# Optimization experiments

Measured on AMD Instinct MI355X. Metric: run time of the kernel, lower is better.

Reference implementation:

```python
import jax, jax.numpy as jnp
import numpy as np
from jax import lax

# sRGB linear -> LMS matrix (Oklab M1)
M1 = jnp.array([[0.4122214708, 0.5363325363, 0.0514459929],
                [0.2119034982, 0.6806995451, 0.1073969566],
                [0.0883024619, 0.2817188376, 0.6299787005]], dtype=jnp.float32)
# LMS^(1/3) -> Oklab matrix (Oklab M2)
M2 = jnp.array([[0.2104542553, 0.7936177850, -0.0040720468],
                [1.9779984951, -2.4285922050, 0.4505937099],
                [0.0259040371, 0.7827717662, -0.8086757660]], dtype=jnp.float32)
_SX = jnp.array([[-1., 0., 1.], [-2., 0., 2.], [-1., 0., 1.]], dtype=jnp.float32)
_SY = jnp.array([[-1., -2., -1.], [0., 0., 0.], [1., 2., 1.]], dtype=jnp.float32)
SOBEL = jnp.stack([_SX, _SY])[:, None]  # (2,1,3,3) cross-correlation kernels

CLOSING_KERNEL = 11
CLOSING_PAD = CLOSING_KERNEL // 2
EDGE_THRESHOLD = 0.5
POST_DILATION = 2
EPS = 0.01


def _srgb_to_linear(srgb):
    srgb = jnp.clip(srgb, 0.0, 1.0)
    return jnp.where(srgb <= 0.04045, srgb / 12.92, ((srgb + 0.055) / 1.055) ** 2.4)


def _rgb_to_oklab(rgb):  # [B,3,H,W] -> [B,3,H,W]
    linear = _srgb_to_linear(rgb)
    lms = jnp.einsum('oc,bchw->bohw', M1, linear)
    lms = jnp.clip(lms, 1e-10, None) ** (1.0 / 3.0)
    return jnp.einsum('oc,bchw->bohw', M2, lms)


def _max_pool(x, k, p):  # torch max_pool2d pads with -inf implicitly
    return lax.reduce_window(x, -jnp.inf, lax.max, (1, 1, k, k), (1, 1, 1, 1),
                             [(0, 0), (0, 0), (p, p), (p, p)])


def _min_pool(x, k, p):  # -max_pool(-x): padding becomes +inf
    return lax.reduce_window(x, jnp.inf, lax.min, (1, 1, k, k), (1, 1, 1, 1),
                             [(0, 0), (0, 0), (p, p), (p, p)])


def _omni_edge(img):  # [B,C,H,W] -> [B,1,H,W]
    B, C, H, W = img.shape
    flat = img.reshape(B * C, 1, H, W)
    g = lax.conv_general_dilated(flat, SOBEL, (1, 1), [(1, 1), (1, 1)])  # [B*C,2,H,W]
    grad = (jnp.abs(g[:, 0]) + jnp.abs(g[:, 1])).reshape(B, C, H, W)
    return jnp.max(grad, axis=1, keepdims=True)


def _crevice_mask(target):
    edge_soft = jnp.clip(_omni_edge(target) / EDGE_THRESHOLD, 0.0, 1.0)
    dilated = _max_pool(edge_soft, CLOSING_KERNEL, CLOSING_PAD)
    closed = _min_pool(dilated, CLOSING_KERNEL, CLOSING_PAD)
    mask = jax.nn.relu(closed - edge_soft)
    if POST_DILATION > 0:
        dk = 2 * POST_DILATION + 1
        mask = _max_pool(mask, dk, POST_DILATION)
    return mask


def setup_inputs() -> dict:
    key = jax.random.key(0)
    k1, k2 = jax.random.split(key)
    shape = (8, 3, 1024, 1024)
    pred = jax.random.uniform(k1, shape, dtype=jnp.float32)
    target = jax.random.uniform(k2, shape, dtype=jnp.float32)
    return {"pred": pred, "target": target}


def reference(pred, target):
    crevice_mask = _crevice_mask(target)
    mask_sum = jnp.maximum(crevice_mask.sum(), 1.0)
    pred_lab = _rgb_to_oklab(pred)
    target_lab = _rgb_to_oklab(target)
    p_a, p_b = pred_lab[:, 1:2], pred_lab[:, 2:3]
    t_a, t_b = target_lab[:, 1:2], target_lab[:, 2:3]
    C_pred = jnp.sqrt(p_a ** 2 + p_b ** 2 + 1e-12)
    C_gt = jnp.sqrt(t_a ** 2 + t_b ** 2 + 1e-12)
    chroma_loss = (jnp.abs(C_pred - C_gt) * crevice_mask).sum() / mask_sum
    dot_ab = p_a * t_a + p_b * t_b
    cos_hue_diff = jnp.clip(dot_ab / (C_pred * C_gt + 1e-12), -1.0, 1.0)
    hue_loss = (jnp.clip(C_gt, EPS, None) * (1.0 - cos_hue_diff) * crevice_mask).sum() / mask_sum
    return chroma_loss + 2.0 * hue_loss
```

## Files before the change

### kernel.cpp

```cpp
#include <hip/hip_runtime.h>
#include <math.h>

#define K1_NR 8
#define SROWS 64
#define PCH   16
#define QCAP  1024


__device__ __forceinline__ float srgb_to_linear(float x) {
    x = fminf(fmaxf(x, 0.0f), 1.0f);
    return (x <= 0.04045f) ? x * (1.0f / 12.92f)
                           : powf((x + 0.055f) * (1.0f / 1.055f), 2.4f);
}

__device__ __forceinline__ void oklab_ab(float r, float g, float b,
                                         float& A, float& Bc) {
    r = srgb_to_linear(r);
    g = srgb_to_linear(g);
    b = srgb_to_linear(b);
    float l = 0.4122214708f * r + 0.5363325363f * g + 0.0514459929f * b;
    float m = 0.2119034982f * r + 0.6806995451f * g + 0.1073969566f * b;
    float s = 0.0883024619f * r + 0.2817188376f * g + 0.6299787005f * b;
    l = cbrtf(fmaxf(l, 1e-10f));
    m = cbrtf(fmaxf(m, 1e-10f));
    s = cbrtf(fmaxf(s, 1e-10f));
    A  = 1.9779984951f * l - 2.428592205f * m + 0.4505937099f * s;
    Bc = 0.0259040371f * l + 0.7827717662f * m - 0.808675766f  * s;
}

__device__ __forceinline__ void color_terms(const float* __restrict__ pred,
                                            const float* __restrict__ target,
                                            size_t off, size_t HWp, float m,
                                            float& sc, float& sh) {
    float pa, pb, ta, tb;
    oklab_ab(pred[off], pred[off + HWp], pred[off + 2 * HWp], pa, pb);
    oklab_ab(target[off], target[off + HWp], target[off + 2 * HWp], ta, tb);
    float Cp = sqrtf(pa * pa + pb * pb + 1e-12f);
    float Cg = sqrtf(ta * ta + tb * tb + 1e-12f);
    sc += fabsf(Cp - Cg) * m;
    float cosd = (pa * ta + pb * tb) / (Cp * Cg + 1e-12f);
    cosd = fminf(fmaxf(cosd, -1.0f), 1.0f);
    sh += fmaxf(Cg, 0.01f) * (1.0f - cosd) * m;
}


__global__ __launch_bounds__(256) void k1_edge(const float* __restrict__ target,
                                               float* __restrict__ edge,
                                               int H, int W) {
    int strips = H / K1_NR;
    int b   = blockIdx.x / strips;
    int ysi = blockIdx.x % strips;
    int lane = threadIdx.x & 63, q = threadIdx.x >> 6;
    int col0 = (q << 8) + (lane << 2);
    int y0 = ysi * K1_NR;
    size_t HW = (size_t)H * W;
    const float* tb = target + (size_t)b * 3 * HW;
    float* ep = edge + (size_t)b * HW + col0;

    bool lok = (col0 > 0);
    bool rok = (col0 + 4 < W);
    int lc = lok ? col0 - 1 : 0;
    int rc = rok ? col0 + 4 : W - 1;

    float4 pr[3], cu[3], nx[3];
    float lpr[3], lcu[3], lnx[3], rpr[3], rcu[3], rnx[3];
#pragma unroll
    for (int c = 0; c < 3; ++c) {
        const float* p = tb + (size_t)c * HW;
        if (y0 > 0) {
            const float* r = p + (size_t)(y0 - 1) * W;
            pr[c]  = *(const float4*)(r + col0);
            lpr[c] = lok ? r[lc] : 0.f;
            rpr[c] = rok ? r[rc] : 0.f;
        } else {
            pr[c] = make_float4(0.f, 0.f, 0.f, 0.f);
            lpr[c] = 0.f; rpr[c] = 0.f;
        }
        const float* r = p + (size_t)y0 * W;
        cu[c]  = *(const float4*)(r + col0);
        lcu[c] = lok ? r[lc] : 0.f;
        rcu[c] = rok ? r[rc] : 0.f;
    }

#pragma unroll
    for (int y = y0; y < y0 + K1_NR; ++y) {
        bool okn = (y + 1 < H);
#pragma unroll
        for (int c = 0; c < 3; ++c) {
            const float* r = tb + (size_t)c * HW + (size_t)(y + 1) * W;
            nx[c]  = okn ? *(const float4*)(r + col0)
                         : make_float4(0.f, 0.f, 0.f, 0.f);
            lnx[c] = (okn && lok) ? r[lc] : 0.f;
            rnx[c] = (okn && rok) ? r[rc] : 0.f;
        }
        float4 g = make_float4(0.f, 0.f, 0.f, 0.f);
#pragma unroll
        for (int c = 0; c < 3; ++c) {
            float4 u, v;
            u.x = fmaf(2.f, cu[c].x, pr[c].x) + nx[c].x;
            u.y = fmaf(2.f, cu[c].y, pr[c].y) + nx[c].y;
            u.z = fmaf(2.f, cu[c].z, pr[c].z) + nx[c].z;
            u.w = fmaf(2.f, cu[c].w, pr[c].w) + nx[c].w;
            v.x = nx[c].x - pr[c].x;
            v.y = nx[c].y - pr[c].y;
            v.z = nx[c].z - pr[c].z;
            v.w = nx[c].w - pr[c].w;
            float ul = fmaf(2.f, lcu[c], lpr[c]) + lnx[c];
            float vl = lnx[c] - lpr[c];
            float ur = fmaf(2.f, rcu[c], rpr[c]) + rnx[c];
            float vr = rnx[c] - rpr[c];
            float4 gx, gy;
            gx.x = u.y - ul;  gx.y = u.z - u.x;
            gx.z = u.w - u.y; gx.w = ur - u.z;
            gy.x = fmaf(2.f, v.x, vl)  + v.y;
            gy.y = fmaf(2.f, v.y, v.x) + v.z;
            gy.z = fmaf(2.f, v.z, v.y) + v.w;
            gy.w = fmaf(2.f, v.w, v.z) + vr;
            g.x = fmaxf(g.x, fabsf(gx.x) + fabsf(gy.x));
            g.y = fmaxf(g.y, fabsf(gx.y) + fabsf(gy.y));
            g.z = fmaxf(g.z, fabsf(gx.z) + fabsf(gy.z));
            g.w = fmaxf(g.w, fabsf(gx.w) + fabsf(gy.w));
        }
        float4 e;
        e.x = fminf(2.f * g.x, 1.f);
        e.y = fminf(2.f * g.y, 1.f);
        e.z = fminf(2.f * g.z, 1.f);
        e.w = fminf(2.f * g.w, 1.f);
        *(float4*)(ep + (size_t)y * W) = e;
#pragma unroll
        for (int c = 0; c < 3; ++c) {
            pr[c] = cu[c];   cu[c] = nx[c];
            lpr[c] = lcu[c]; lcu[c] = lnx[c];
            rpr[c] = rcu[c]; rcu[c] = rnx[c];
        }
    }
}


template <int R, bool ISMAX, bool SUB_EDGE>
__global__ __launch_bounds__(256) void pool_kernel(const float* __restrict__ in,
                                                   const float* __restrict__ edge,
                                                   float* __restrict__ out,
                                                   int H, int W) {
    const int OUTW = 256 - 2 * R;
    __shared__ float s_v[PCH][256];
    int cb = (W + OUTW - 1) / OUTW;
    int rs = H / SROWS;
    int blk = blockIdx.x;
    int b   = blk / (cb * rs);
    int t   = blk % (cb * rs);
    int bxi = t / rs, ysi = t % rs;
    int tid = threadIdx.x;
    int col = bxi * OUTW - R + tid;
    int cc  = min(max(col, 0), W - 1);
    size_t base = (size_t)b * H * W;
    const float* colp = in + base + cc;
    int ys = ysi * SROWS;
    bool writer = (tid >= R) && (tid < OUTW + R) && (col < W);

    for (int ph = 0; ph < SROWS / PCH; ++ph) {
        int y0 = ys + ph * PCH;
        float w[PCH + 2 * R];
#pragma unroll
        for (int k = 0; k < PCH + 2 * R; ++k) {
            int r = min(max(y0 - R + k, 0), H - 1);
            w[k] = colp[(size_t)r * W];
        }
        float v[PCH];
#pragma unroll
        for (int k = 0; k < PCH; ++k) {
            float m = w[k];
#pragma unroll
            for (int d = 1; d <= 2 * R; ++d)
                m = ISMAX ? fmaxf(m, w[k + d]) : fminf(m, w[k + d]);
            v[k] = m;
        }
        __syncthreads();
#pragma unroll
        for (int k = 0; k < PCH; ++k) s_v[k][tid] = v[k];
        __syncthreads();
        if (writer) {
#pragma unroll
            for (int k = 0; k < PCH; ++k) {
                float m = s_v[k][tid - R];
#pragma unroll
                for (int d = 1; d <= 2 * R; ++d)
                    m = ISMAX ? fmaxf(m, s_v[k][tid - R + d])
                              : fminf(m, s_v[k][tid - R + d]);
                size_t gi = base + (size_t)(y0 + k) * W + col;
                out[gi] = SUB_EDGE ? fmaxf(m - edge[gi], 0.f) : m;
            }
        }
    }
}


__global__ __launch_bounds__(256) void k4_loss(const float* __restrict__ pred,
                                               const float* __restrict__ target,
                                               const float* __restrict__ mask0,
                                               float* __restrict__ partials,
                                               int H, int W, int nb) {
    const int R = 2, OUTW = 256 - 2 * R;
    __shared__ float s_v[PCH][256];
    __shared__ int   q_pos[QCAP];
    __shared__ float q_m[QCAP];
    __shared__ int   cnt;
    __shared__ float s_red[3][4];

    int cb = (W + OUTW - 1) / OUTW;
    int rs = H / SROWS;
    int blk = blockIdx.x;
    int b   = blk / (cb * rs);
    int t   = blk % (cb * rs);
    int bxi = t / rs, ysi = t % rs;
    int tid = threadIdx.x;
    int col = bxi * OUTW - R + tid;
    int cc  = min(max(col, 0), W - 1);
    size_t HWp  = (size_t)H * W;
    size_t base = (size_t)b * HWp;
    size_t cbase = (size_t)b * 3 * HWp;
    const float* colp = mask0 + base + cc;
    int ys = ysi * SROWS;
    bool writer = (tid >= R) && (tid < OUTW + R) && (col < W);

    float sm = 0.f, sc = 0.f, sh = 0.f;

    for (int ph = 0; ph < SROWS / PCH; ++ph) {
        int y0 = ys + ph * PCH;
        float w[PCH + 2 * R];
#pragma unroll
        for (int k = 0; k < PCH + 2 * R; ++k) {
            int r = min(max(y0 - R + k, 0), H - 1);
            w[k] = colp[(size_t)r * W];
        }
        float v[PCH];
#pragma unroll
        for (int k = 0; k < PCH; ++k) {
            float m = w[k];
#pragma unroll
            for (int d = 1; d <= 2 * R; ++d) m = fmaxf(m, w[k + d]);
            v[k] = m;
        }
        __syncthreads();
#pragma unroll
        for (int k = 0; k < PCH; ++k) s_v[k][tid] = v[k];
        if (tid == 0) cnt = 0;
        __syncthreads();
        if (writer) {
#pragma unroll
            for (int k = 0; k < PCH; ++k) {
                float m = s_v[k][tid - R];
#pragma unroll
                for (int d = 1; d <= 2 * R; ++d)
                    m = fmaxf(m, s_v[k][tid - R + d]);
                sm += m;
                if (m > 0.f) {
                    int pos = atomicAdd(&cnt, 1);
                    if (pos < QCAP) {
                        q_pos[pos] = ((y0 + k) << 16) | col;
                        q_m[pos] = m;
                    } else {
                        color_terms(pred, target,
                                    cbase + (size_t)(y0 + k) * W + col,
                                    HWp, m, sc, sh);
                    }
                }
            }
        }
        __syncthreads();
        int n = min(cnt, QCAP);
        for (int i = tid; i < n; i += 256) {
            int pk = q_pos[i];
            color_terms(pred, target,
                        cbase + (size_t)(pk >> 16) * W + (pk & 0xffff),
                        HWp, q_m[i], sc, sh);
        }
    }

#pragma unroll
    for (int off = 32; off > 0; off >>= 1) {
        sm += __shfl_down(sm, off);
        sc += __shfl_down(sc, off);
        sh += __shfl_down(sh, off);
    }
    int lane = tid & 63, wav = tid >> 6;
    __syncthreads();
    if (lane == 0) { s_red[0][wav] = sm; s_red[1][wav] = sc; s_red[2][wav] = sh; }
    __syncthreads();
    if (tid == 0) {
        float tm = 0, tc = 0, th = 0;
        for (int i = 0; i < 4; ++i) {
            tm += s_red[0][i]; tc += s_red[1][i]; th += s_red[2][i];
        }
        partials[blk]          = tm;
        partials[nb + blk]     = tc;
        partials[2 * nb + blk] = th;
    }
}

__global__ void finalize_kernel(const float* __restrict__ partials, int nb,
                                float* __restrict__ out) {
    double sm = 0.0, sc = 0.0, sh = 0.0;
    for (int i = threadIdx.x; i < nb; i += blockDim.x) {
        sm += (double)partials[i];
        sc += (double)partials[nb + i];
        sh += (double)partials[2 * nb + i];
    }
    __shared__ double red[3][256];
    red[0][threadIdx.x] = sm;
    red[1][threadIdx.x] = sc;
    red[2][threadIdx.x] = sh;
    __syncthreads();
    for (int s = blockDim.x / 2; s > 0; s >>= 1) {
        if ((int)threadIdx.x < s) {
            red[0][threadIdx.x] += red[0][threadIdx.x + s];
            red[1][threadIdx.x] += red[1][threadIdx.x + s];
            red[2][threadIdx.x] += red[2][threadIdx.x + s];
        }
        __syncthreads();
    }
    if (threadIdx.x == 0) {
        double ms = fmax(red[0][0], 1.0);
        out[0] = (float)(red[1][0] / ms + 2.0 * red[2][0] / ms);
    }
}


extern "C" void kernel_launch(void* const* d_in, const int* in_sizes, int n_in,
                              void* d_out, int out_size, void* d_ws, size_t ws_size,
                              hipStream_t stream) {
    const float* pred   = (const float*)d_in[0];
    const float* target = (const float*)d_in[1];
    float* out = (float*)d_out;

    const int H = 1024, W = 1024;
    int Bn = in_sizes[0] / (3 * H * W);
    size_t plane = (size_t)Bn * H * W * sizeof(float);

    char* ws = (char*)d_ws;
    float* planeA = (float*)ws;
    float* planeB = (float*)(ws + plane);
    float* partials = (float*)(ws + 2 * plane);

    int g1 = Bn * (H / K1_NR);
    int rs = H / SROWS;
    int cbP = (W + 245) / 246;
    int cb4 = (W + 251) / 252;
    int gP = Bn * cbP * rs;
    int g4 = Bn * cb4 * rs;

    k1_edge<<<g1, 256, 0, stream>>>(target, planeA, H, W);
    pool_kernel<5, true, false><<<gP, 256, 0, stream>>>(planeA, nullptr, planeB, H, W);
    pool_kernel<5, false, true><<<gP, 256, 0, stream>>>(planeB, planeA, planeA, H, W);
    k4_loss<<<g4, 256, 0, stream>>>(pred, target, planeA, partials, H, W, g4);
    finalize_kernel<<<1, 256, 0, stream>>>(partials, g4, out);
}
```

Measured before the change: 92.73 us.

## Skew channel rows in Sobel edge kernel and double rows per block

Rewrites the Sobel edge kernel so the three colour channels are processed on staggered rows. At each step, channel c works on row s-c, and per-channel gradient maxima are carried in rolling accumulators, with each output row written two steps later. Rows per block go from 8 to 16, which cuts the share of redundant halo-row loads. The aim is to spread the concurrent memory streams across channel planes and amortise halo traffic. In exchange the main loop is no longer unrolled, gains per-channel branches, and launches fewer blocks.

```diff
diff --git a/kernel.cpp b/kernel.cpp
--- a/kernel.cpp
+++ b/kernel.cpp
@@ -1,7 +1,7 @@
 #include <hip/hip_runtime.h>
 #include <math.h>
 
-#define K1_NR 8
+#define K1_NR 16
 #define SROWS 64
 #define PCH   16
 #define QCAP  1024
@@ -44,15 +44,55 @@
 }
 
 
+__device__ __forceinline__ void k1_load_row(const float* __restrict__ tb,
+                                            size_t HW, int c, int r,
+                                            int H, int W, int col0,
+                                            bool lok, bool rok, int lc, int rc,
+                                            float4& m4, float& ml, float& mr) {
+    if (r >= 0 && r < H) {
+        const float* rp = tb + (size_t)c * HW + (size_t)r * W;
+        m4 = *(const float4*)(rp + col0);
+        ml = lok ? rp[lc] : 0.f;
+        mr = rok ? rp[rc] : 0.f;
+    } else {
+        m4 = make_float4(0.f, 0.f, 0.f, 0.f);
+        ml = 0.f; mr = 0.f;
+    }
+}
+
+__device__ __forceinline__ float4 k1_sobel_g(const float4& pr, const float4& cu,
+                                             const float4& nx,
+                                             float lpr, float lcu, float lnx,
+                                             float rpr, float rcu, float rnx) {
+    float4 u, v;
+    u.x = fmaf(2.f, cu.x, pr.x) + nx.x;
+    u.y = fmaf(2.f, cu.y, pr.y) + nx.y;
+    u.z = fmaf(2.f, cu.z, pr.z) + nx.z;
+    u.w = fmaf(2.f, cu.w, pr.w) + nx.w;
+    v.x = nx.x - pr.x; v.y = nx.y - pr.y;
+    v.z = nx.z - pr.z; v.w = nx.w - pr.w;
+    float ul = fmaf(2.f, lcu, lpr) + lnx;
+    float vl = lnx - lpr;
+    float ur = fmaf(2.f, rcu, rpr) + rnx;
+    float vr = rnx - rpr;
+    float4 g;
+    g.x = fabsf(u.y - ul)  + fabsf(fmaf(2.f, v.x, vl) + v.y);
+    g.y = fabsf(u.z - u.x) + fabsf(fmaf(2.f, v.y, v.x) + v.z);
+    g.z = fabsf(u.w - u.y) + fabsf(fmaf(2.f, v.z, v.y) + v.w);
+    g.w = fabsf(ur - u.z)  + fabsf(fmaf(2.f, v.w, v.z) + vr);
+    return g;
+}
+
 __global__ __launch_bounds__(256) void k1_edge(const float* __restrict__ target,
                                                float* __restrict__ edge,
                                                int H, int W) {
     int strips = H / K1_NR;
     int b   = blockIdx.x / strips;
     int ysi = blockIdx.x % strips;
-    int lane = threadIdx.x & 63, q = threadIdx.x >> 6;
-    int col0 = (q << 8) + (lane << 2);
+    int t   = threadIdx.x;
+    int col0 = t << 2;
     int y0 = ysi * K1_NR;
+    int yend = y0 + K1_NR - 1;
     size_t HW = (size_t)H * W;
     const float* tb = target + (size_t)b * 3 * HW;
     float* ep = edge + (size_t)b * HW + col0;
@@ -62,77 +102,54 @@
     int lc = lok ? col0 - 1 : 0;
     int rc = rok ? col0 + 4 : W - 1;
 
-    float4 pr[3], cu[3], nx[3];
-    float lpr[3], lcu[3], lnx[3], rpr[3], rcu[3], rnx[3];
+    float4 pr[3], cu[3];
+    float lpr[3], lcu[3], rpr[3], rcu[3];
 #pragma unroll
     for (int c = 0; c < 3; ++c) {
-        const float* p = tb + (size_t)c * HW;
-        if (y0 > 0) {
-            const float* r = p + (size_t)(y0 - 1) * W;
-            pr[c]  = *(const float4*)(r + col0);
-            lpr[c] = lok ? r[lc] : 0.f;
-            rpr[c] = rok ? r[rc] : 0.f;
-        } else {
-            pr[c] = make_float4(0.f, 0.f, 0.f, 0.f);
-            lpr[c] = 0.f; rpr[c] = 0.f;
-        }
-        const float* r = p + (size_t)y0 * W;
-        cu[c]  = *(const float4*)(r + col0);
-        lcu[c] = lok ? r[lc] : 0.f;
-        rcu[c] = rok ? r[rc] : 0.f;
-    }
-
-#pragma unroll
-    for (int y = y0; y < y0 + K1_NR; ++y) {
-        bool okn = (y + 1 < H);
+        k1_load_row(tb, HW, c, y0 - c - 1, H, W, col0, lok, rok, lc, rc,
+                    pr[c], lpr[c], rpr[c]);
+        k1_load_row(tb, HW, c, y0 - c, H, W, col0, lok, rok, lc, rc,
+                    cu[c], lcu[c], rcu[c]);
+    }
+
+    float4 acc1 = make_float4(0.f, 0.f, 0.f, 0.f);
+    float4 acc2 = make_float4(0.f, 0.f, 0.f, 0.f);
+
+    for (int s = y0; s < y0 + K1_NR + 2; ++s) {
+        float4 g0 = make_float4(0.f, 0.f, 0.f, 0.f);
 #pragma unroll
         for (int c = 0; c < 3; ++c) {
-            const float* r = tb + (size_t)c * HW + (size_t)(y + 1) * W;
-            nx[c]  = okn ? *(const float4*)(r + col0)
-                         : make_float4(0.f, 0.f, 0.f, 0.f);
-            lnx[c] = (okn && lok) ? r[lc] : 0.f;
-            rnx[c] = (okn && rok) ? r[rc] : 0.f;
-        }
-        float4 g = make_float4(0.f, 0.f, 0.f, 0.f);
-#pragma unroll
-        for (int c = 0; c < 3; ++c) {
-            float4 u, v;
-            u.x = fmaf(2.f, cu[c].x, pr[c].x) + nx[c].x;
-            u.y = fmaf(2.f, cu[c].y, pr[c].y) + nx[c].y;
-            u.z = fmaf(2.f, cu[c].z, pr[c].z) + nx[c].z;
-            u.w = fmaf(2.f, cu[c].w, pr[c].w) + nx[c].w;
-            v.x = nx[c].x - pr[c].x;
-            v.y = nx[c].y - pr[c].y;
-            v.z = nx[c].z - pr[c].z;
-            v.w = nx[c].w - pr[c].w;
-            float ul = fmaf(2.f, lcu[c], lpr[c]) + lnx[c];
-            float vl = lnx[c] - lpr[c];
-            float ur = fmaf(2.f, rcu[c], rpr[c]) + rnx[c];
-            float vr = rnx[c] - rpr[c];
-            float4 gx, gy;
-            gx.x = u.y - ul;  gx.y = u.z - u.x;
-            gx.z = u.w - u.y; gx.w = ur - u.z;
-            gy.x = fmaf(2.f, v.x, vl)  + v.y;
-            gy.y = fmaf(2.f, v.y, v.x) + v.z;
-            gy.z = fmaf(2.f, v.z, v.y) + v.w;
-            gy.w = fmaf(2.f, v.w, v.z) + vr;
-            g.x = fmaxf(g.x, fabsf(gx.x) + fabsf(gy.x));
-            g.y = fmaxf(g.y, fabsf(gx.y) + fabsf(gy.y));
-            g.z = fmaxf(g.z, fabsf(gx.z) + fabsf(gy.z));
-            g.w = fmaxf(g.w, fabsf(gx.w) + fabsf(gy.w));
-        }
-        float4 e;
-        e.x = fminf(2.f * g.x, 1.f);
-        e.y = fminf(2.f * g.y, 1.f);
-        e.z = fminf(2.f * g.z, 1.f);
-        e.w = fminf(2.f * g.w, 1.f);
-        *(float4*)(ep + (size_t)y * W) = e;
-#pragma unroll
-        for (int c = 0; c < 3; ++c) {
-            pr[c] = cu[c];   cu[c] = nx[c];
-            lpr[c] = lcu[c]; lcu[c] = lnx[c];
-            rpr[c] = rcu[c]; rcu[c] = rnx[c];
-        }
+            if (s - c <= yend) {
+                float4 nx; float lnx, rnx;
+                k1_load_row(tb, HW, c, s - c + 1, H, W, col0, lok, rok, lc, rc,
+                            nx, lnx, rnx);
+                float4 g = k1_sobel_g(pr[c], cu[c], nx,
+                                      lpr[c], lcu[c], lnx,
+                                      rpr[c], rcu[c], rnx);
+                if (c == 0) {
+                    g0 = g;
+                } else if (c == 1) {
+                    acc1.x = fmaxf(acc1.x, g.x); acc1.y = fmaxf(acc1.y, g.y);
+                    acc1.z = fmaxf(acc1.z, g.z); acc1.w = fmaxf(acc1.w, g.w);
+                } else {
+                    acc2.x = fmaxf(acc2.x, g.x); acc2.y = fmaxf(acc2.y, g.y);
+                    acc2.z = fmaxf(acc2.z, g.z); acc2.w = fmaxf(acc2.w, g.w);
+                }
+                pr[c] = cu[c]; cu[c] = nx;
+                lpr[c] = lcu[c]; lcu[c] = lnx;
+                rpr[c] = rcu[c]; rcu[c] = rnx;
+            }
+        }
+        if (s >= y0 + 2) {
+            float4 e;
+            e.x = fminf(2.f * acc2.x, 1.f);
+            e.y = fminf(2.f * acc2.y, 1.f);
+            e.z = fminf(2.f * acc2.z, 1.f);
+            e.w = fminf(2.f * acc2.w, 1.f);
+            *(float4*)(ep + (size_t)(s - 2) * W) = e;
+        }
+        acc2 = acc1;
+        acc1 = g0;
     }
 }
 
```

New measurement: 101.0 us. +8.9%, slower.
